# Optimization experiments

Measured on AMD Instinct MI355X. Metric: run time of the kernel, lower is better.

The kernel has to match this reference:

```python
import jax, jax.numpy as jnp
import numpy as np

BATCH = 4096
LATENT = 2048
ZDIM = 128
TEMP = 0.5
PRIOR = 0.3
PRIOR_PRIME = 0.5
GAMMA = 1.0
BETA = 0.0
EPS = 1e-8  # torch CosineSimilarity eps


def setup_inputs() -> dict:
    key = jax.random.key(0)
    k = jax.random.split(key, 6)
    return {
        "h_i": jax.random.normal(k[0], (BATCH, LATENT), dtype=jnp.float32),
        "h_j": jax.random.normal(k[1], (BATCH, LATENT), dtype=jnp.float32),
        "z_i": jax.random.normal(k[2], (BATCH, ZDIM), dtype=jnp.float32),
        "z_j": jax.random.normal(k[3], (BATCH, ZDIM), dtype=jnp.float32),
        "target": jax.random.randint(k[4], (BATCH, 1), 0, 2, dtype=jnp.int64 if jax.config.jax_enable_x64 else jnp.int32),
        "W": jax.random.normal(k[5], (1, LATENT), dtype=jnp.float32) * (1.0 / np.sqrt(LATENT)),
        "b": jnp.zeros((1,), dtype=jnp.float32),
        "weight_onnpu": jnp.asarray(0.5, dtype=jnp.float32),
    }


def _onnpu_loss(inp, target):
    # inp: [B, 1] classifier logit; target: [B, 1] in {0, 1} -> {-1, +1}
    t = (target * 2 - 1).astype(inp.dtype)
    positive = (t == 1).astype(inp.dtype)
    unlabeled = (t == -1).astype(inp.dtype)
    one = jnp.asarray(1.0, inp.dtype)
    n_pos = jnp.maximum(one, jnp.sum(positive))
    n_unl = jnp.maximum(one, jnp.sum(unlabeled))
    sig = jax.nn.sigmoid  # loss(x) = sigmoid(-x)
    y_pos = sig(-(positive * inp)) * positive
    y_pos_inv = sig(positive * inp) * positive
    y_unl = sig(unlabeled * inp) * unlabeled
    positive_risk = PRIOR_PRIME / n_pos * jnp.sum(y_pos)
    negative_risk = ((1.0 - PRIOR_PRIME) / (n_unl * (1.0 - PRIOR)) * jnp.sum(y_unl)
                     - (1.0 - PRIOR_PRIME) * PRIOR / (n_pos * (1.0 - PRIOR)) * jnp.sum(y_pos_inv))
    # nnPU correction (nnPU=True, beta=0, gamma=1)
    return jnp.where(negative_risk < -BETA, -GAMMA * negative_risk,
                     positive_risk + negative_risk)


def _nt_xent_loss(z_i, z_j):
    B = z_i.shape[0]
    N = 2 * B
    z = jnp.concatenate([z_i, z_j], axis=0)  # [N, D]
    zn = z / jnp.maximum(jnp.linalg.norm(z, axis=1, keepdims=True), EPS)
    sim = (zn @ zn.T) / TEMP  # [N, N] cosine similarity / temperature
    idx = jnp.arange(N)
    pos = sim[idx, (idx + B) % N]  # positive pair logit per row
    # CE over [positive | all-other-than-self]: denominator is logsumexp over
    # the row with the self-similarity (diagonal) excluded.
    sim_masked = jnp.where(idx[:, None] == idx[None, :], -jnp.inf, sim)
    lse = jax.nn.logsumexp(sim_masked, axis=1)
    return jnp.sum(lse - pos) / N


def reference(h_i, h_j, z_i, z_j, target, W, b, weight_onnpu):
    logit_i = h_i @ W.T + b  # [B, 1]
    logit_j = h_j @ W.T + b
    onnpu_l = 0.5 * (_onnpu_loss(logit_i, target) + _onnpu_loss(logit_j, target))
    nt_xent_l = _nt_xent_loss(z_i, z_j)
    return weight_onnpu * onnpu_l + (1.0 - weight_onnpu) * nt_xent_l
```

## Files before the change

kernel.cpp:

```cpp
#include <hip/hip_runtime.h>

#define BATCH  4096
#define NROWS  8192
#define LATENT 2048
#define ZDIM   128
#define PRIORc       0.3f
#define PRIOR_PRIMEc 0.5f

typedef __attribute__((ext_vector_type(8))) short bf16x8;
typedef __attribute__((ext_vector_type(4))) float f32x4;

__device__ inline unsigned short f2bf_rne(float f) {
    unsigned int u = __float_as_uint(f);
    u = u + 0x7fffu + ((u >> 16) & 1u);
    return (unsigned short)(u >> 16);
}

__device__ inline float wave_reduce_sum(float v) {
#pragma unroll
    for (int m = 1; m < 64; m <<= 1) v += __shfl_xor(v, m, 64);
    return v;
}

__global__ void k_znorm(const float* __restrict__ z_i, const float* __restrict__ z_j,
                        unsigned short* __restrict__ znb) {
    int wave = threadIdx.x >> 6, lane = threadIdx.x & 63;
    int r = blockIdx.x * 4 + wave;
    const float* zr = (r < BATCH) ? (z_i + (size_t)r * ZDIM)
                                  : (z_j + (size_t)(r - BATCH) * ZDIM);
    float2 v = ((const float2*)zr)[lane];
    float ss = v.x * v.x + v.y * v.y;
    ss = wave_reduce_sum(ss);
    float scale = (1.0f / fmaxf(sqrtf(ss), 1e-8f)) * 1.41421356237f;
    int g = r >> 4, rr = r & 15;
    int kt = lane >> 4;
    int q  = (lane >> 2) & 3;
    int j  = (lane & 3) * 2;
    size_t off = ((size_t)(g * 4 + kt) * 64 + (q * 16 + rr)) * 8 + j;
    ushort2 w2; w2.x = f2bf_rne(v.x * scale); w2.y = f2bf_rne(v.y * scale);
    *(ushort2*)(znb + off) = w2;
}

__global__ void k_logits(const float* __restrict__ h_i, const float* __restrict__ h_j,
                         const float* __restrict__ W, const float* __restrict__ b,
                         float* __restrict__ logits) {
    int wave = threadIdx.x >> 6, lane = threadIdx.x & 63;
    int r = blockIdx.x * 4 + wave;
    const float* h = (r < BATCH) ? (h_i + (size_t)r * LATENT)
                                 : (h_j + (size_t)(r - BATCH) * LATENT);
    const float4* h4 = (const float4*)h;
    const float4* w4 = (const float4*)W;
    float s = 0.f;
#pragma unroll
    for (int it = 0; it < 8; ++it) {
        float4 a = h4[it * 64 + lane];
        float4 w = w4[it * 64 + lane];
        s += a.x * w.x + a.y * w.y + a.z * w.z + a.w * w.w;
    }
    s = wave_reduce_sum(s);
    if (lane == 0) logits[r] = s + b[0];
}

__global__ void k_onnpu_part(const float* __restrict__ logits, const int* __restrict__ target,
                             float* __restrict__ acc8) {
    int r = blockIdx.x * 256 + threadIdx.x;
    float li = logits[r], lj = logits[BATCH + r];
    int t = target[r];
    bool pos = (t == 1);
    float v[8];
    v[0] = pos ? 1.f : 0.f;
    v[1] = pos ? 0.f : 1.f;
    v[2] = pos ? 1.f / (1.f + __expf(li)) : 0.f;
    v[3] = pos ? 1.f / (1.f + __expf(-li)) : 0.f;
    v[4] = pos ? 0.f : 1.f / (1.f + __expf(-li));
    v[5] = pos ? 1.f / (1.f + __expf(lj)) : 0.f;
    v[6] = pos ? 1.f / (1.f + __expf(-lj)) : 0.f;
    v[7] = pos ? 0.f : 1.f / (1.f + __expf(-lj));
    int lane = threadIdx.x & 63;
#pragma unroll
    for (int i = 0; i < 8; ++i) {
        float s = wave_reduce_sum(v[i]);
        if (lane == 0) atomicAdd(&acc8[i], s);
    }
}

__global__ void __launch_bounds__(256, 3) k_sim(const unsigned short* __restrict__ znb,
                                                float* __restrict__ S_row) {
    int lane = threadIdx.x & 63, wave = threadIdx.x >> 6;
    int q = lane >> 4, t = lane & 15;
    int row0 = blockIdx.x * 128 + (wave >> 1) * 64;
    int gA = row0 >> 4;
    const bf16x8* zf = (const bf16x8*)znb;

    bf16x8 a[4][4];
#pragma unroll
    for (int mt = 0; mt < 4; ++mt)
#pragma unroll
        for (int kt = 0; kt < 4; ++kt)
            a[mt][kt] = zf[(size_t)((gA + mt) * 4 + kt) * 64 + lane];

    float s[16];
#pragma unroll
    for (int i = 0; i < 16; ++i) s[i] = 0.f;

    int colbase = blockIdx.y * 512 + (wave & 1) * 64;
#pragma unroll 1
    for (int it = 0; it < 4; ++it) {
        int col0 = colbase + it * 128;
        int gB = col0 >> 4;
#pragma unroll
        for (int nt = 0; nt < 4; ++nt) {
            bf16x8 b[4];
#pragma unroll
            for (int kt = 0; kt < 4; ++kt)
                b[kt] = zf[(size_t)((gB + nt) * 4 + kt) * 64 + lane];
            f32x4 acc[4];
            f32x4 zero = {0.f, 0.f, 0.f, 0.f};
#pragma unroll
            for (int mt = 0; mt < 4; ++mt) acc[mt] = zero;
#pragma unroll
            for (int kt = 0; kt < 4; ++kt)
#pragma unroll
                for (int mt = 0; mt < 4; ++mt)
                    acc[mt] = __builtin_amdgcn_mfma_f32_16x16x32_bf16(a[mt][kt], b[kt], acc[mt], 0, 0, 0);
            int gcol = col0 + nt * 16 + t;
#pragma unroll
            for (int mt = 0; mt < 4; ++mt) {
                int rowb = row0 + mt * 16 + q * 4;
#pragma unroll
                for (int reg = 0; reg < 4; ++reg) {
                    float e = __expf(acc[mt][reg]);
                    s[mt * 4 + reg] += (rowb + reg == gcol) ? 0.f : e;
                }
            }
        }
    }
#pragma unroll
    for (int i = 0; i < 16; ++i) {
        float v = s[i];
        v += __shfl_xor(v, 1, 64);
        v += __shfl_xor(v, 2, 64);
        v += __shfl_xor(v, 4, 64);
        v += __shfl_xor(v, 8, 64);
        if (t == 0) atomicAdd(&S_row[row0 + (i >> 2) * 16 + q * 4 + (i & 3)], v);
    }
}

__global__ void k_pos(const float* __restrict__ z_i, const float* __restrict__ z_j,
                      float* __restrict__ pos) {
    int wave = threadIdx.x >> 6, lane = threadIdx.x & 63;
    int r = blockIdx.x * 4 + wave;
    int p = (r + BATCH) & (NROWS - 1);
    const float* zr = (r < BATCH) ? (z_i + (size_t)r * ZDIM)
                                  : (z_j + (size_t)(r - BATCH) * ZDIM);
    const float* zp = (p < BATCH) ? (z_i + (size_t)p * ZDIM)
                                  : (z_j + (size_t)(p - BATCH) * ZDIM);
    float2 a = ((const float2*)zr)[lane];
    float2 c = ((const float2*)zp)[lane];
    float d = a.x * c.x + a.y * c.y;
    float sr = a.x * a.x + a.y * a.y;
    float sp = c.x * c.x + c.y * c.y;
    d = wave_reduce_sum(d);
    sr = wave_reduce_sum(sr);
    sp = wave_reduce_sum(sp);
    if (lane == 0)
        pos[r] = 2.0f * d / (fmaxf(sqrtf(sr), 1e-8f) * fmaxf(sqrtf(sp), 1e-8f));
}

__global__ void k_final(const float* __restrict__ S_row, const float* __restrict__ pos,
                        const float* __restrict__ acc8, const float* __restrict__ w_onnpu,
                        float* __restrict__ out) {
    float s = 0.f;
    for (int r = threadIdx.x; r < NROWS; r += 1024)
        s += __logf(S_row[r]) - pos[r];
    __shared__ float red[16];
    int wave = threadIdx.x >> 6, lane = threadIdx.x & 63;
    s = wave_reduce_sum(s);
    if (lane == 0) red[wave] = s;
    __syncthreads();
    if (threadIdx.x == 0) {
        float tot = 0.f;
#pragma unroll
        for (int i = 0; i < 16; ++i) tot += red[i];
        float ntxent = tot / (float)NROWS;
        float np = fmaxf(1.f, acc8[0]), nu = fmaxf(1.f, acc8[1]);
        float pr_i = PRIOR_PRIMEc / np * acc8[2];
        float nr_i = (1.f - PRIOR_PRIMEc) / (nu * (1.f - PRIORc)) * acc8[4]
                   - (1.f - PRIOR_PRIMEc) * PRIORc / (np * (1.f - PRIORc)) * acc8[3];
        float li_loss = (nr_i < 0.f) ? -nr_i : (pr_i + nr_i);
        float pr_j = PRIOR_PRIMEc / np * acc8[5];
        float nr_j = (1.f - PRIOR_PRIMEc) / (nu * (1.f - PRIORc)) * acc8[7]
                   - (1.f - PRIOR_PRIMEc) * PRIORc / (np * (1.f - PRIORc)) * acc8[6];
        float lj_loss = (nr_j < 0.f) ? -nr_j : (pr_j + nr_j);
        float onnpu = 0.5f * (li_loss + lj_loss);
        float w = w_onnpu[0];
        out[0] = w * onnpu + (1.f - w) * ntxent;
    }
}

extern "C" void kernel_launch(void* const* d_in, const int* in_sizes, int n_in,
                              void* d_out, int out_size, void* d_ws, size_t ws_size,
                              hipStream_t stream) {
    const float* h_i = (const float*)d_in[0];
    const float* h_j = (const float*)d_in[1];
    const float* z_i = (const float*)d_in[2];
    const float* z_j = (const float*)d_in[3];
    const int* target = (const int*)d_in[4];
    const float* W = (const float*)d_in[5];
    const float* b = (const float*)d_in[6];
    const float* w_onnpu = (const float*)d_in[7];

    char* ws = (char*)d_ws;
    unsigned short* znb = (unsigned short*)ws;
    float* logits = (float*)(ws + 2097152);
    float* S_row  = (float*)(ws + 2097152 + 32768);
    float* acc8   = (float*)(ws + 2097152 + 65536);
    float* pos    = (float*)(ws + 2097152 + 65536 + 256);
    float* out = (float*)d_out;

    hipMemsetAsync(S_row, 0, 32768 + 256, stream);
    k_znorm<<<2048, 256, 0, stream>>>(z_i, z_j, znb);
    k_logits<<<2048, 256, 0, stream>>>(h_i, h_j, W, b, logits);
    k_onnpu_part<<<16, 256, 0, stream>>>(logits, target, acc8);
    dim3 g(64, 16);
    k_sim<<<g, 256, 0, stream>>>(znb, S_row);
    k_pos<<<2048, 256, 0, stream>>>(z_i, z_j, pos);
    k_final<<<1, 1024, 0, stream>>>(S_row, pos, acc8, w_onnpu, out);
}
```

Measured before the change: 149.0 us.

## Fuse kernels: merge znorm with pos, co-schedule sim and logits, fold onnpu into final

The normalization and positive-pair kernels are merged so each wave handles an i/j pair, writing both bf16 rows and both pos entries at once. The similarity GEMM and the memory-bound logits GEMV now run as one launch with disjoint block ranges, so the bandwidth-heavy h reads can overlap the MFMA/exp work. The onnpu partial reduction moves into the final single-block kernel, which drops the atomics and one launch. The sim loop also prefetches the next B fragment while computing the current one, which adds register pressure under launch bounds of 3 blocks per CU.

```diff
diff --git a/kernel.cpp b/kernel.cpp
--- a/kernel.cpp
+++ b/kernel.cpp
@@ -22,175 +22,189 @@
     return v;
 }
 
-__global__ void k_znorm(const float* __restrict__ z_i, const float* __restrict__ z_j,
-                        unsigned short* __restrict__ znb) {
+__global__ void k_zprep(const float* __restrict__ z_i, const float* __restrict__ z_j,
+                        unsigned short* __restrict__ znb, float* __restrict__ pos) {
     int wave = threadIdx.x >> 6, lane = threadIdx.x & 63;
     int r = blockIdx.x * 4 + wave;
-    const float* zr = (r < BATCH) ? (z_i + (size_t)r * ZDIM)
-                                  : (z_j + (size_t)(r - BATCH) * ZDIM);
-    float2 v = ((const float2*)zr)[lane];
-    float ss = v.x * v.x + v.y * v.y;
-    ss = wave_reduce_sum(ss);
-    float scale = (1.0f / fmaxf(sqrtf(ss), 1e-8f)) * 1.41421356237f;
-    int g = r >> 4, rr = r & 15;
+    int p = r + BATCH;
+    float2 a = ((const float2*)(z_i + (size_t)r * ZDIM))[lane];
+    float2 c = ((const float2*)(z_j + (size_t)r * ZDIM))[lane];
+    float sa = a.x * a.x + a.y * a.y;
+    float sc = c.x * c.x + c.y * c.y;
+    float dd = a.x * c.x + a.y * c.y;
+    sa = wave_reduce_sum(sa);
+    sc = wave_reduce_sum(sc);
+    dd = wave_reduce_sum(dd);
+    float inva = 1.f / fmaxf(sqrtf(sa), 1e-8f);
+    float invc = 1.f / fmaxf(sqrtf(sc), 1e-8f);
+    if (lane == 0) {
+        float pv = 2.0f * dd * inva * invc;
+        pos[r] = pv;
+        pos[p] = pv;
+    }
     int kt = lane >> 4;
     int q  = (lane >> 2) & 3;
     int j  = (lane & 3) * 2;
-    size_t off = ((size_t)(g * 4 + kt) * 64 + (q * 16 + rr)) * 8 + j;
-    ushort2 w2; w2.x = f2bf_rne(v.x * scale); w2.y = f2bf_rne(v.y * scale);
-    *(ushort2*)(znb + off) = w2;
-}
-
-__global__ void k_logits(const float* __restrict__ h_i, const float* __restrict__ h_j,
-                         const float* __restrict__ W, const float* __restrict__ b,
-                         float* __restrict__ logits) {
+    int lrow = q * 16;
+    float fa = inva * 1.41421356237f, fc = invc * 1.41421356237f;
+    {
+        size_t off = ((size_t)((r >> 4) * 4 + kt) * 64 + (lrow + (r & 15))) * 8 + j;
+        ushort2 w2; w2.x = f2bf_rne(a.x * fa); w2.y = f2bf_rne(a.y * fa);
+        *(ushort2*)(znb + off) = w2;
+    }
+    {
+        size_t off = ((size_t)((p >> 4) * 4 + kt) * 64 + (lrow + (p & 15))) * 8 + j;
+        ushort2 w2; w2.x = f2bf_rne(c.x * fc); w2.y = f2bf_rne(c.y * fc);
+        *(ushort2*)(znb + off) = w2;
+    }
+}
+
+__global__ void __launch_bounds__(256, 3) k_mega(
+        const unsigned short* __restrict__ znb, float* __restrict__ S_row,
+        const float* __restrict__ h_i, const float* __restrict__ h_j,
+        const float* __restrict__ W, const float* __restrict__ bb,
+        float* __restrict__ logits) {
+    int bid = blockIdx.x;
+    int lane = threadIdx.x & 63, wave = threadIdx.x >> 6;
+    if (bid < 1024) {
+        int q = lane >> 4, t = lane & 15;
+        int row0 = (bid & 63) * 128 + (wave >> 1) * 64;
+        int gA = row0 >> 4;
+        const bf16x8* zf = (const bf16x8*)znb;
+
+        bf16x8 a[4][4];
+#pragma unroll
+        for (int mt = 0; mt < 4; ++mt)
+#pragma unroll
+            for (int kt = 0; kt < 4; ++kt)
+                a[mt][kt] = zf[(size_t)((gA + mt) * 4 + kt) * 64 + lane];
+
+        float s[16];
+#pragma unroll
+        for (int i = 0; i < 16; ++i) s[i] = 0.f;
+
+        int colbase = (bid >> 6) * 512 + (wave & 1) * 64;
+        int cb4 = colbase >> 4;
+        bf16x8 b[4];
+#pragma unroll
+        for (int kt = 0; kt < 4; ++kt)
+            b[kt] = zf[(size_t)(cb4 * 4 + kt) * 64 + lane];
+
+#pragma unroll 1
+        for (int it = 0; it < 4; ++it) {
+#pragma unroll
+            for (int nt = 0; nt < 4; ++nt) {
+                bf16x8 bn[4];
+                if (!(it == 3 && nt == 3)) {
+                    int ng = cb4 + (nt == 3 ? (it + 1) * 8 : it * 8 + nt + 1);
+#pragma unroll
+                    for (int kt = 0; kt < 4; ++kt)
+                        bn[kt] = zf[(size_t)(ng * 4 + kt) * 64 + lane];
+                }
+                f32x4 acc[4];
+                f32x4 zero = {0.f, 0.f, 0.f, 0.f};
+#pragma unroll
+                for (int mt = 0; mt < 4; ++mt) acc[mt] = zero;
+#pragma unroll
+                for (int kt = 0; kt < 4; ++kt)
+#pragma unroll
+                    for (int mt = 0; mt < 4; ++mt)
+                        acc[mt] = __builtin_amdgcn_mfma_f32_16x16x32_bf16(a[mt][kt], b[kt], acc[mt], 0, 0, 0);
+                int gcol = colbase + it * 128 + nt * 16 + t;
+#pragma unroll
+                for (int mt = 0; mt < 4; ++mt) {
+                    int rowb = row0 + mt * 16 + q * 4;
+#pragma unroll
+                    for (int reg = 0; reg < 4; ++reg) {
+                        float e = __expf(acc[mt][reg]);
+                        s[mt * 4 + reg] += (rowb + reg == gcol) ? 0.f : e;
+                    }
+                }
+#pragma unroll
+                for (int kt = 0; kt < 4; ++kt) b[kt] = bn[kt];
+            }
+        }
+#pragma unroll
+        for (int i = 0; i < 16; ++i) {
+            float v = s[i];
+            v += __shfl_xor(v, 1, 64);
+            v += __shfl_xor(v, 2, 64);
+            v += __shfl_xor(v, 4, 64);
+            v += __shfl_xor(v, 8, 64);
+            if (t == 0) atomicAdd(&S_row[row0 + (i >> 2) * 16 + q * 4 + (i & 3)], v);
+        }
+    } else {
+        int r = (bid - 1024) * 4 + wave;
+        const float* h = (r < BATCH) ? (h_i + (size_t)r * LATENT)
+                                     : (h_j + (size_t)(r - BATCH) * LATENT);
+        const float4* h4 = (const float4*)h;
+        const float4* w4 = (const float4*)W;
+        float s = 0.f;
+#pragma unroll
+        for (int itr = 0; itr < 8; ++itr) {
+            float4 av = h4[itr * 64 + lane];
+            float4 wv = w4[itr * 64 + lane];
+            s += av.x * wv.x + av.y * wv.y + av.z * wv.z + av.w * wv.w;
+        }
+        s = wave_reduce_sum(s);
+        if (lane == 0) logits[r] = s + bb[0];
+    }
+}
+
+__global__ void k_final(const float* __restrict__ S_row, const float* __restrict__ pos,
+                        const float* __restrict__ logits, const int* __restrict__ target,
+                        const float* __restrict__ w_onnpu, float* __restrict__ out) {
+    float nt_s = 0.f;
+    for (int r = threadIdx.x; r < NROWS; r += 1024)
+        nt_s += __logf(S_row[r]) - pos[r];
+    float v[8];
+#pragma unroll
+    for (int i = 0; i < 8; ++i) v[i] = 0.f;
+    for (int r = threadIdx.x; r < BATCH; r += 1024) {
+        float li = logits[r], lj = logits[BATCH + r];
+        bool p = (target[r] == 1);
+        float si_n = 1.f / (1.f + __expf(li));
+        float si_p = 1.f / (1.f + __expf(-li));
+        float sj_n = 1.f / (1.f + __expf(lj));
+        float sj_p = 1.f / (1.f + __expf(-lj));
+        v[0] += p ? 1.f : 0.f;
+        v[1] += p ? 0.f : 1.f;
+        v[2] += p ? si_n : 0.f;
+        v[3] += p ? si_p : 0.f;
+        v[4] += p ? 0.f : si_p;
+        v[5] += p ? sj_n : 0.f;
+        v[6] += p ? sj_p : 0.f;
+        v[7] += p ? 0.f : sj_p;
+    }
+    __shared__ float red[16][9];
     int wave = threadIdx.x >> 6, lane = threadIdx.x & 63;
-    int r = blockIdx.x * 4 + wave;
-    const float* h = (r < BATCH) ? (h_i + (size_t)r * LATENT)
-                                 : (h_j + (size_t)(r - BATCH) * LATENT);
-    const float4* h4 = (const float4*)h;
-    const float4* w4 = (const float4*)W;
-    float s = 0.f;
-#pragma unroll
-    for (int it = 0; it < 8; ++it) {
-        float4 a = h4[it * 64 + lane];
-        float4 w = w4[it * 64 + lane];
-        s += a.x * w.x + a.y * w.y + a.z * w.z + a.w * w.w;
-    }
-    s = wave_reduce_sum(s);
-    if (lane == 0) logits[r] = s + b[0];
-}
-
-__global__ void k_onnpu_part(const float* __restrict__ logits, const int* __restrict__ target,
-                             float* __restrict__ acc8) {
-    int r = blockIdx.x * 256 + threadIdx.x;
-    float li = logits[r], lj = logits[BATCH + r];
-    int t = target[r];
-    bool pos = (t == 1);
-    float v[8];
-    v[0] = pos ? 1.f : 0.f;
-    v[1] = pos ? 0.f : 1.f;
-    v[2] = pos ? 1.f / (1.f + __expf(li)) : 0.f;
-    v[3] = pos ? 1.f / (1.f + __expf(-li)) : 0.f;
-    v[4] = pos ? 0.f : 1.f / (1.f + __expf(-li));
-    v[5] = pos ? 1.f / (1.f + __expf(lj)) : 0.f;
-    v[6] = pos ? 1.f / (1.f + __expf(-lj)) : 0.f;
-    v[7] = pos ? 0.f : 1.f / (1.f + __expf(-lj));
-    int lane = threadIdx.x & 63;
-#pragma unroll
-    for (int i = 0; i < 8; ++i) {
-        float s = wave_reduce_sum(v[i]);
-        if (lane == 0) atomicAdd(&acc8[i], s);
-    }
-}
-
-__global__ void __launch_bounds__(256, 3) k_sim(const unsigned short* __restrict__ znb,
-                                                float* __restrict__ S_row) {
-    int lane = threadIdx.x & 63, wave = threadIdx.x >> 6;
-    int q = lane >> 4, t = lane & 15;
-    int row0 = blockIdx.x * 128 + (wave >> 1) * 64;
-    int gA = row0 >> 4;
-    const bf16x8* zf = (const bf16x8*)znb;
-
-    bf16x8 a[4][4];
-#pragma unroll
-    for (int mt = 0; mt < 4; ++mt)
-#pragma unroll
-        for (int kt = 0; kt < 4; ++kt)
-            a[mt][kt] = zf[(size_t)((gA + mt) * 4 + kt) * 64 + lane];
-
-    float s[16];
-#pragma unroll
-    for (int i = 0; i < 16; ++i) s[i] = 0.f;
-
-    int colbase = blockIdx.y * 512 + (wave & 1) * 64;
-#pragma unroll 1
-    for (int it = 0; it < 4; ++it) {
-        int col0 = colbase + it * 128;
-        int gB = col0 >> 4;
-#pragma unroll
-        for (int nt = 0; nt < 4; ++nt) {
-            bf16x8 b[4];
-#pragma unroll
-            for (int kt = 0; kt < 4; ++kt)
-                b[kt] = zf[(size_t)((gB + nt) * 4 + kt) * 64 + lane];
-            f32x4 acc[4];
-            f32x4 zero = {0.f, 0.f, 0.f, 0.f};
-#pragma unroll
-            for (int mt = 0; mt < 4; ++mt) acc[mt] = zero;
-#pragma unroll
-            for (int kt = 0; kt < 4; ++kt)
-#pragma unroll
-                for (int mt = 0; mt < 4; ++mt)
-                    acc[mt] = __builtin_amdgcn_mfma_f32_16x16x32_bf16(a[mt][kt], b[kt], acc[mt], 0, 0, 0);
-            int gcol = col0 + nt * 16 + t;
-#pragma unroll
-            for (int mt = 0; mt < 4; ++mt) {
-                int rowb = row0 + mt * 16 + q * 4;
-#pragma unroll
-                for (int reg = 0; reg < 4; ++reg) {
-                    float e = __expf(acc[mt][reg]);
-                    s[mt * 4 + reg] += (rowb + reg == gcol) ? 0.f : e;
-                }
-            }
-        }
-    }
-#pragma unroll
-    for (int i = 0; i < 16; ++i) {
-        float v = s[i];
-        v += __shfl_xor(v, 1, 64);
-        v += __shfl_xor(v, 2, 64);
-        v += __shfl_xor(v, 4, 64);
-        v += __shfl_xor(v, 8, 64);
-        if (t == 0) atomicAdd(&S_row[row0 + (i >> 2) * 16 + q * 4 + (i & 3)], v);
-    }
-}
-
-__global__ void k_pos(const float* __restrict__ z_i, const float* __restrict__ z_j,
-                      float* __restrict__ pos) {
-    int wave = threadIdx.x >> 6, lane = threadIdx.x & 63;
-    int r = blockIdx.x * 4 + wave;
-    int p = (r + BATCH) & (NROWS - 1);
-    const float* zr = (r < BATCH) ? (z_i + (size_t)r * ZDIM)
-                                  : (z_j + (size_t)(r - BATCH) * ZDIM);
-    const float* zp = (p < BATCH) ? (z_i + (size_t)p * ZDIM)
-                                  : (z_j + (size_t)(p - BATCH) * ZDIM);
-    float2 a = ((const float2*)zr)[lane];
-    float2 c = ((const float2*)zp)[lane];
-    float d = a.x * c.x + a.y * c.y;
-    float sr = a.x * a.x + a.y * a.y;
-    float sp = c.x * c.x + c.y * c.y;
-    d = wave_reduce_sum(d);
-    sr = wave_reduce_sum(sr);
-    sp = wave_reduce_sum(sp);
-    if (lane == 0)
-        pos[r] = 2.0f * d / (fmaxf(sqrtf(sr), 1e-8f) * fmaxf(sqrtf(sp), 1e-8f));
-}
-
-__global__ void k_final(const float* __restrict__ S_row, const float* __restrict__ pos,
-                        const float* __restrict__ acc8, const float* __restrict__ w_onnpu,
-                        float* __restrict__ out) {
-    float s = 0.f;
-    for (int r = threadIdx.x; r < NROWS; r += 1024)
-        s += __logf(S_row[r]) - pos[r];
-    __shared__ float red[16];
-    int wave = threadIdx.x >> 6, lane = threadIdx.x & 63;
-    s = wave_reduce_sum(s);
-    if (lane == 0) red[wave] = s;
+    nt_s = wave_reduce_sum(nt_s);
+#pragma unroll
+    for (int i = 0; i < 8; ++i) v[i] = wave_reduce_sum(v[i]);
+    if (lane == 0) {
+        red[wave][0] = nt_s;
+#pragma unroll
+        for (int i = 0; i < 8; ++i) red[wave][1 + i] = v[i];
+    }
     __syncthreads();
     if (threadIdx.x == 0) {
-        float tot = 0.f;
-#pragma unroll
-        for (int i = 0; i < 16; ++i) tot += red[i];
-        float ntxent = tot / (float)NROWS;
-        float np = fmaxf(1.f, acc8[0]), nu = fmaxf(1.f, acc8[1]);
-        float pr_i = PRIOR_PRIMEc / np * acc8[2];
-        float nr_i = (1.f - PRIOR_PRIMEc) / (nu * (1.f - PRIORc)) * acc8[4]
-                   - (1.f - PRIOR_PRIMEc) * PRIORc / (np * (1.f - PRIORc)) * acc8[3];
+        float t[9];
+#pragma unroll
+        for (int i = 0; i < 9; ++i) {
+            float acc = 0.f;
+#pragma unroll
+            for (int wv = 0; wv < 16; ++wv) acc += red[wv][i];
+            t[i] = acc;
+        }
+        float ntxent = t[0] / (float)NROWS;
+        float np = fmaxf(1.f, t[1]), nu = fmaxf(1.f, t[2]);
+        float pr_i = PRIOR_PRIMEc / np * t[3];
+        float nr_i = (1.f - PRIOR_PRIMEc) / (nu * (1.f - PRIORc)) * t[5]
+                   - (1.f - PRIOR_PRIMEc) * PRIORc / (np * (1.f - PRIORc)) * t[4];
         float li_loss = (nr_i < 0.f) ? -nr_i : (pr_i + nr_i);
-        float pr_j = PRIOR_PRIMEc / np * acc8[5];
-        float nr_j = (1.f - PRIOR_PRIMEc) / (nu * (1.f - PRIORc)) * acc8[7]
-                   - (1.f - PRIOR_PRIMEc) * PRIORc / (np * (1.f - PRIORc)) * acc8[6];
+        float pr_j = PRIOR_PRIMEc / np * t[6];
+        float nr_j = (1.f - PRIOR_PRIMEc) / (nu * (1.f - PRIORc)) * t[8]
+                   - (1.f - PRIOR_PRIMEc) * PRIORc / (np * (1.f - PRIORc)) * t[7];
         float lj_loss = (nr_j < 0.f) ? -nr_j : (pr_j + nr_j);
         float onnpu = 0.5f * (li_loss + lj_loss);
         float w = w_onnpu[0];
@@ -212,18 +226,13 @@
 
     char* ws = (char*)d_ws;
     unsigned short* znb = (unsigned short*)ws;
-    float* logits = (float*)(ws + 2097152);
-    float* S_row  = (float*)(ws + 2097152 + 32768);
-    float* acc8   = (float*)(ws + 2097152 + 65536);
-    float* pos    = (float*)(ws + 2097152 + 65536 + 256);
+    float* S_row  = (float*)(ws + 2097152);
+    float* pos    = (float*)(ws + 2097152 + 32768);
+    float* logits = (float*)(ws + 2097152 + 65536);
     float* out = (float*)d_out;
 
-    hipMemsetAsync(S_row, 0, 32768 + 256, stream);
-    k_znorm<<<2048, 256, 0, stream>>>(z_i, z_j, znb);
-    k_logits<<<2048, 256, 0, stream>>>(h_i, h_j, W, b, logits);
-    k_onnpu_part<<<16, 256, 0, stream>>>(logits, target, acc8);
-    dim3 g(64, 16);
-    k_sim<<<g, 256, 0, stream>>>(znb, S_row);
-    k_pos<<<2048, 256, 0, stream>>>(z_i, z_j, pos);
-    k_final<<<1, 1024, 0, stream>>>(S_row, pos, acc8, w_onnpu, out);
-}
+    hipMemsetAsync(S_row, 0, 32768, stream);
+    k_zprep<<<1024, 256, 0, stream>>>(z_i, z_j, znb, pos);
+    k_mega<<<3072, 256, 0, stream>>>(znb, S_row, h_i, h_j, W, b, logits);
+    k_final<<<1, 1024, 0, stream>>>(S_row, pos, logits, target, w_onnpu, out);
+}
```

Measured after the change: 136.2 us. -8.6%, faster.
